# Optimization experiments

Hardware: AMD Instinct MI355X
Metric: run time of the kernel (lower is better)

## Reference

```python
import jax, jax.numpy as jnp
import numpy as np


def setup_inputs() -> dict:
    key = jax.random.key(0)
    k1, k2 = jax.random.split(key)
    num_tokens, top_k, num_experts = 1048576, 8, 64
    top_scores = jax.random.uniform(k1, (num_tokens, top_k), dtype=jnp.float32)
    selected_experts_indices = jax.random.randint(
        k2, (num_tokens, top_k), 0, num_experts, dtype=jnp.int64
    ) if jax.config.jax_enable_x64 else jax.random.randint(
        k2, (num_tokens, top_k), 0, num_experts, dtype=jnp.int32
    )
    return {
        "top_scores": top_scores,
        "selected_experts_indices": selected_experts_indices,
        "num_experts": num_experts,
    }


def reference(top_scores, selected_experts_indices, num_experts):
    flat_idx = selected_experts_indices.reshape(-1)  # [num_tokens*top_k]
    # histogram of tokens per expert (torch.histc returns float)
    num_tokens_per_expert = jnp.bincount(flat_idx, length=num_experts).astype(jnp.float32)
    # stable argsort by expert id -> permutation grouping tokens by expert
    token_indices_experts_sorted = jnp.argsort(flat_idx, stable=True)
    # gather routing scores into expert-sorted order
    top_scores_experts_sorted = top_scores.reshape(-1)[token_indices_experts_sorted]
    return (
        top_scores_experts_sorted,
        token_indices_experts_sorted,
        num_tokens_per_expert,
    )
```

## Files before the change

### kernel.cpp

```cpp
#include <hip/hip_runtime.h>


#define TILE 4096
#define WCH  1024
#define RND  16

__device__ __forceinline__ unsigned long long match_mask(
    unsigned key,
    unsigned long long b0, unsigned long long b1, unsigned long long b2,
    unsigned long long b3, unsigned long long b4, unsigned long long b5,
    unsigned long long am) {
  unsigned long long m = am;
  m &= (key & 1u)  ? b0 : ~b0;
  m &= (key & 2u)  ? b1 : ~b1;
  m &= (key & 4u)  ? b2 : ~b2;
  m &= (key & 8u)  ? b3 : ~b3;
  m &= (key & 16u) ? b4 : ~b4;
  m &= (key & 32u) ? b5 : ~b5;
  return m;
}

__global__ __launch_bounds__(256) void hist_kernel(
    const int* __restrict__ idx, unsigned* __restrict__ countsT,
    int N, int nb) {
  __shared__ unsigned h[4][64];
  const int wave = threadIdx.x >> 6;
  const int lane = threadIdx.x & 63;

  long long base = (long long)blockIdx.x * TILE;
  long long rem = (long long)N - base;
  unsigned cnt = 0;

  if (rem >= TILE) {
    const int4* v = (const int4*)(idx + base);
    unsigned es[16];
    #pragma unroll
    for (int k = 0; k < 4; ++k) {
      int4 x = v[threadIdx.x + k * 256];
      es[k * 4 + 0] = ((unsigned)x.x) & 63u;
      es[k * 4 + 1] = ((unsigned)x.y) & 63u;
      es[k * 4 + 2] = ((unsigned)x.z) & 63u;
      es[k * 4 + 3] = ((unsigned)x.w) & 63u;
    }
    #pragma unroll
    for (int r = 0; r < 16; ++r) {
      unsigned e = es[r];
      unsigned long long b0 = __ballot(e & 1u);
      unsigned long long b1 = __ballot(e & 2u);
      unsigned long long b2 = __ballot(e & 4u);
      unsigned long long b3 = __ballot(e & 8u);
      unsigned long long b4 = __ballot(e & 16u);
      unsigned long long b5 = __ballot(e & 32u);
      cnt += (unsigned)__popcll(
          match_mask((unsigned)lane, b0, b1, b2, b3, b4, b5, ~0ull));
    }
  } else {
    long long wstart = base + (long long)wave * WCH;
    for (int r = 0; r < RND; ++r) {
      long long i = wstart + (long long)r * 64 + lane;
      bool valid = i < (long long)N;
      unsigned long long am = __ballot(valid ? 1 : 0);
      unsigned e = valid ? (((unsigned)idx[i]) & 63u) : 0u;
      unsigned long long b0 = __ballot(e & 1u);
      unsigned long long b1 = __ballot(e & 2u);
      unsigned long long b2 = __ballot(e & 4u);
      unsigned long long b3 = __ballot(e & 8u);
      unsigned long long b4 = __ballot(e & 16u);
      unsigned long long b5 = __ballot(e & 32u);
      cnt += (unsigned)__popcll(
          match_mask((unsigned)lane, b0, b1, b2, b3, b4, b5, am));
    }
  }

  h[wave][lane] = cnt;
  __syncthreads();
  if (threadIdx.x < 64) {
    countsT[(size_t)blockIdx.x * 64 + threadIdx.x] =
        h[0][threadIdx.x] + h[1][threadIdx.x] + h[2][threadIdx.x] + h[3][threadIdx.x];
  }
}

__global__ __launch_bounds__(256) void scan_kernel(
    unsigned* __restrict__ countsT, unsigned* __restrict__ totals,
    float* __restrict__ out_counts, int nb) {
  const int e = blockIdx.x;
  const int t = threadIdx.x;
  const int wave = t >> 6;
  const int lane = t & 63;

  __shared__ unsigned buf[2048];
  __shared__ unsigned wsum[4];

  unsigned carry = 0;
  for (int c = 0; c < nb; c += 2048) {
    int m = nb - c; if (m > 2048) m = 2048;
    for (int j = t; j < 2048; j += 256)
      buf[j] = (j < m) ? countsT[(size_t)(c + j) * 64 + e] : 0u;
    __syncthreads();
    unsigned v[8]; unsigned s = 0;
    #pragma unroll
    for (int k = 0; k < 8; ++k) { v[k] = buf[t * 8 + k]; s += v[k]; }
    unsigned inc = s;
    #pragma unroll
    for (int d = 1; d < 64; d <<= 1) {
      unsigned nv = __shfl_up(inc, d, 64);
      if (lane >= d) inc += nv;
    }
    if (lane == 63) wsum[wave] = inc;
    __syncthreads();
    unsigned woff = 0;
    for (int w = 0; w < wave; ++w) woff += wsum[w];
    unsigned btot = wsum[0] + wsum[1] + wsum[2] + wsum[3];
    unsigned run = carry + woff + (inc - s);
    #pragma unroll
    for (int k = 0; k < 8; ++k) { buf[t * 8 + k] = run; run += v[k]; }
    __syncthreads();
    for (int j = t; j < 2048; j += 256)
      if (j < m) countsT[(size_t)(c + j) * 64 + e] = buf[j];
    carry += btot;
    __syncthreads();
  }
  if (t == 0) {
    totals[e] = carry;
    out_counts[e] = (float)carry;
  }
}

__global__ __launch_bounds__(256, 4) void scatter_kernel(
    const int* __restrict__ idx, const float* __restrict__ scores,
    const unsigned* __restrict__ baseT, const unsigned* __restrict__ totals,
    float* __restrict__ out_scores, float* __restrict__ out_idx,
    int N, int nb) {
  __shared__ __align__(16) uint2 sdat[TILE];
  __shared__ __align__(16) unsigned char tmpb[4][64][RND];
  __shared__ unsigned shc[4][64];
  __shared__ unsigned gdest[64];

  const int t = threadIdx.x;
  const int wave = t >> 6;
  const int lane = t & 63;
  const unsigned long long lt = (1ull << lane) - 1ull;

  const long long base = (long long)blockIdx.x * TILE;
  const long long start = base + (long long)wave * WCH;
  const bool fullt = (base + TILE) <= (long long)N;

  const unsigned tot = totals[lane];
  const unsigned gb0 = baseT[(size_t)blockIdx.x * 64 + lane];

  unsigned e_pk[4] = {0, 0, 0, 0};
  unsigned r_pk[4] = {0, 0, 0, 0};
  float    sreg[RND];
  unsigned c_pk[4];
  unsigned wtotal = 0;

  unsigned* idxs = (unsigned*)sdat;

  if (fullt) {
    {
      const int4* gi = (const int4*)(idx + base);
      int4 a0 = gi[t];
      int4 a1 = gi[t + 256];
      int4 a2 = gi[t + 512];
      int4 a3 = gi[t + 768];
      #pragma unroll
      for (int r = 0; r < RND; ++r) sreg[r] = scores[start + r * 64 + lane];
      ((int4*)idxs)[t] = a0;
      ((int4*)idxs)[t + 256] = a1;
      ((int4*)idxs)[t + 512] = a2;
      ((int4*)idxs)[t + 768] = a3;
    }
    *(uint4*)(&tmpb[wave][lane][0]) = make_uint4(0u, 0u, 0u, 0u);
    __syncthreads();

    #pragma unroll
    for (int r = 0; r < RND; ++r) {
      unsigned e = idxs[wave * WCH + r * 64 + lane] & 63u;
      unsigned long long b0 = __ballot(e & 1u);
      unsigned long long b1 = __ballot(e & 2u);
      unsigned long long b2 = __ballot(e & 4u);
      unsigned long long b3 = __ballot(e & 8u);
      unsigned long long b4 = __ballot(e & 16u);
      unsigned long long b5 = __ballot(e & 32u);
      unsigned long long ms = match_mask(e, b0, b1, b2, b3, b4, b5, ~0ull);
      unsigned rank = (unsigned)__popcll(ms & lt);
      unsigned rcnt = (unsigned)__popcll(ms);
      if (rank == 0) tmpb[wave][e][r] = (unsigned char)rcnt;
      const int q = r >> 2, sh = (r & 3) * 8;
      e_pk[q] |= e << sh;
      r_pk[q] |= rank << sh;
    }
    uint4 cw = *(const uint4*)(&tmpb[wave][lane][0]);
    c_pk[0] = cw.x; c_pk[1] = cw.y; c_pk[2] = cw.z; c_pk[3] = cw.w;
  } else {
    for (int j = t; j < TILE; j += 256) sdat[j].y = 0xFFFFFFFFu;
    *(uint4*)(&tmpb[wave][lane][0]) = make_uint4(0u, 0u, 0u, 0u);
    __syncthreads();
    for (int r = 0; r < RND; ++r) {
      long long i = start + (long long)r * 64 + lane;
      bool valid = i < (long long)N;
      unsigned long long am = __ballot(valid ? 1 : 0);
      unsigned e = valid ? (((unsigned)idx[i]) & 63u) : 0u;
      sreg[r] = valid ? scores[i] : 0.0f;
      unsigned long long b0 = __ballot(e & 1u);
      unsigned long long b1 = __ballot(e & 2u);
      unsigned long long b2 = __ballot(e & 4u);
      unsigned long long b3 = __ballot(e & 8u);
      unsigned long long b4 = __ballot(e & 16u);
      unsigned long long b5 = __ballot(e & 32u);
      unsigned long long ms = match_mask(e, b0, b1, b2, b3, b4, b5, am);
      unsigned rank = (unsigned)__popcll(ms & lt);
      unsigned rcnt = (unsigned)__popcll(ms);
      if (valid && rank == 0) tmpb[wave][e][r] = (unsigned char)rcnt;
      const int q = r >> 2, sh = (r & 3) * 8;
      e_pk[q] |= e << sh;
      r_pk[q] |= rank << sh;
    }
    uint4 cw = *(const uint4*)(&tmpb[wave][lane][0]);
    c_pk[0] = cw.x; c_pk[1] = cw.y; c_pk[2] = cw.z; c_pk[3] = cw.w;
  }

  {
    unsigned acc = 0;
    #pragma unroll
    for (int q = 0; q < 4; ++q)
      acc += (c_pk[q] & 0x00FF00FFu) + ((c_pk[q] >> 8) & 0x00FF00FFu);
    wtotal = (acc & 0xFFFFu) + (acc >> 16);
  }

  shc[wave][lane] = wtotal;
  __syncthreads();

  unsigned c0 = shc[0][lane], c1 = shc[1][lane];
  unsigned c2 = shc[2][lane], c3 = shc[3][lane];
  unsigned bt = c0 + c1 + c2 + c3;
  unsigned wpre = 0;
  if (wave > 0) wpre += c0;
  if (wave > 1) wpre += c1;
  if (wave > 2) wpre += c2;

  unsigned s = bt;
  #pragma unroll
  for (int d = 1; d < 64; d <<= 1) {
    unsigned nv = __shfl_up(s, d, 64);
    if (lane >= d) s += nv;
  }
  unsigned bstart = s - bt;
  unsigned wbase = bstart + wpre;

  unsigned cur[RND];
  {
    unsigned acc = wbase;
    #pragma unroll
    for (int r = 0; r < RND; ++r) {
      cur[r] = acc;
      acc += (c_pk[r >> 2] >> ((r & 3) * 8)) & 0xffu;
    }
  }

  if (wave == 0) {
    unsigned s2 = tot;
    #pragma unroll
    for (int d = 1; d < 64; d <<= 1) {
      unsigned nv = __shfl_up(s2, d, 64);
      if (lane >= d) s2 += nv;
    }
    unsigned estart = s2 - tot;
    gdest[lane] = estart + gb0 - bstart;
  }

  if (fullt) {
    #pragma unroll
    for (int r = 0; r < RND; ++r) {
      unsigned i32 = (unsigned)start + r * 64 + lane;
      const int q = r >> 2, sh = (r & 3) * 8;
      unsigned e    = (e_pk[q] >> sh) & 0xffu;
      unsigned rank = (r_pk[q] >> sh) & 0xffu;
      unsigned pos = (unsigned)__shfl((int)cur[r], (int)e, 64) + rank;
      sdat[pos] = make_uint2(__float_as_uint(sreg[r]), (i32 << 6) | e);
    }
  } else {
    for (int r = 0; r < RND; ++r) {
      long long i = start + (long long)r * 64 + lane;
      bool valid = i < (long long)N;
      const int q = r >> 2, sh = (r & 3) * 8;
      unsigned e    = (e_pk[q] >> sh) & 0xffu;
      unsigned rank = (r_pk[q] >> sh) & 0xffu;
      unsigned pos = (unsigned)__shfl((int)cur[r], (int)e, 64) + rank;
      if (valid) {
        sdat[pos] = make_uint2(__float_as_uint(sreg[r]), (((unsigned)i) << 6) | e);
      }
    }
  }
  __syncthreads();

  if (fullt) {
    #pragma unroll
    for (int k = 0; k < TILE / 256; ++k) {
      int j = t + k * 256;
      uint2 v = sdat[j];
      unsigned e = v.y & 63u;
      unsigned d = gdest[e] + (unsigned)j;
      out_scores[d] = __uint_as_float(v.x);
      out_idx[d] = (float)(v.y >> 6);
    }
  } else {
    for (int j = t; j < TILE; j += 256) {
      uint2 v = sdat[j];
      if (v.y == 0xFFFFFFFFu) continue;
      unsigned e = v.y & 63u;
      unsigned d = gdest[e] + (unsigned)j;
      out_scores[d] = __uint_as_float(v.x);
      out_idx[d] = (float)(v.y >> 6);
    }
  }
}

extern "C" void kernel_launch(void* const* d_in, const int* in_sizes, int n_in,
                              void* d_out, int out_size, void* d_ws, size_t ws_size,
                              hipStream_t stream) {
  const float* scores = (const float*)d_in[0];
  const int* idx = (const int*)d_in[1];
  int N = in_sizes[0];

  float* out_scores = (float*)d_out;
  float* out_idx = out_scores + N;
  float* out_counts = out_idx + N;

  int nb = (N + TILE - 1) / TILE;
  unsigned* countsT = (unsigned*)d_ws;
  unsigned* totals = countsT + (size_t)nb * 64;

  hist_kernel<<<nb, 256, 0, stream>>>(idx, countsT, N, nb);
  scan_kernel<<<64, 256, 0, stream>>>(countsT, totals, out_counts, nb);
  scatter_kernel<<<nb, 256, 0, stream>>>(idx, scores, countsT, totals,
                                         out_scores, out_idx, N, nb);
}
```

Before: 139.9 us.

## Gather scores at write-out instead of staging them through shared memory

The scatter kernel no longer preloads scores into registers and stages them next to indices in shared memory. The LDS tile shrinks from uint2 to unsigned per element, and launch bounds rise to 7 blocks per CU for higher occupancy. Scores are now gathered from global memory by source index during the final write-out. This replaces a coalesced score load with a scattered gather, which may cost more memory traffic than the LDS and occupancy savings recover.

Result: slower. 149.1 us (+6.6%).

```diff
diff --git a/kernel.cpp b/kernel.cpp
--- a/kernel.cpp
+++ b/kernel.cpp
@@ -126,12 +126,12 @@
   }
 }
 
-__global__ __launch_bounds__(256, 4) void scatter_kernel(
+__global__ __launch_bounds__(256, 7) void scatter_kernel(
     const int* __restrict__ idx, const float* __restrict__ scores,
     const unsigned* __restrict__ baseT, const unsigned* __restrict__ totals,
     float* __restrict__ out_scores, float* __restrict__ out_idx,
     int N, int nb) {
-  __shared__ __align__(16) uint2 sdat[TILE];
+  __shared__ __align__(16) unsigned sdat[TILE];
   __shared__ __align__(16) unsigned char tmpb[4][64][RND];
   __shared__ unsigned shc[4][64];
   __shared__ unsigned gdest[64];
@@ -150,11 +150,8 @@
 
   unsigned e_pk[4] = {0, 0, 0, 0};
   unsigned r_pk[4] = {0, 0, 0, 0};
-  float    sreg[RND];
   unsigned c_pk[4];
   unsigned wtotal = 0;
-
-  unsigned* idxs = (unsigned*)sdat;
 
   if (fullt) {
     {
@@ -163,19 +160,17 @@
       int4 a1 = gi[t + 256];
       int4 a2 = gi[t + 512];
       int4 a3 = gi[t + 768];
-      #pragma unroll
-      for (int r = 0; r < RND; ++r) sreg[r] = scores[start + r * 64 + lane];
-      ((int4*)idxs)[t] = a0;
-      ((int4*)idxs)[t + 256] = a1;
-      ((int4*)idxs)[t + 512] = a2;
-      ((int4*)idxs)[t + 768] = a3;
+      ((int4*)sdat)[t] = a0;
+      ((int4*)sdat)[t + 256] = a1;
+      ((int4*)sdat)[t + 512] = a2;
+      ((int4*)sdat)[t + 768] = a3;
     }
     *(uint4*)(&tmpb[wave][lane][0]) = make_uint4(0u, 0u, 0u, 0u);
     __syncthreads();
 
     #pragma unroll
     for (int r = 0; r < RND; ++r) {
-      unsigned e = idxs[wave * WCH + r * 64 + lane] & 63u;
+      unsigned e = sdat[wave * WCH + r * 64 + lane] & 63u;
       unsigned long long b0 = __ballot(e & 1u);
       unsigned long long b1 = __ballot(e & 2u);
       unsigned long long b2 = __ballot(e & 4u);
@@ -193,15 +188,15 @@
     uint4 cw = *(const uint4*)(&tmpb[wave][lane][0]);
     c_pk[0] = cw.x; c_pk[1] = cw.y; c_pk[2] = cw.z; c_pk[3] = cw.w;
   } else {
-    for (int j = t; j < TILE; j += 256) sdat[j].y = 0xFFFFFFFFu;
+    for (int j = t; j < TILE; j += 256) sdat[j] = 0xFFFFFFFFu;
     *(uint4*)(&tmpb[wave][lane][0]) = make_uint4(0u, 0u, 0u, 0u);
     __syncthreads();
+    unsigned epk_local[RND];
     for (int r = 0; r < RND; ++r) {
       long long i = start + (long long)r * 64 + lane;
       bool valid = i < (long long)N;
       unsigned long long am = __ballot(valid ? 1 : 0);
       unsigned e = valid ? (((unsigned)idx[i]) & 63u) : 0u;
-      sreg[r] = valid ? scores[i] : 0.0f;
       unsigned long long b0 = __ballot(e & 1u);
       unsigned long long b1 = __ballot(e & 2u);
       unsigned long long b2 = __ballot(e & 4u);
@@ -215,6 +210,7 @@
       const int q = r >> 2, sh = (r & 3) * 8;
       e_pk[q] |= e << sh;
       r_pk[q] |= rank << sh;
+      (void)epk_local;
     }
     uint4 cw = *(const uint4*)(&tmpb[wave][lane][0]);
     c_pk[0] = cw.x; c_pk[1] = cw.y; c_pk[2] = cw.z; c_pk[3] = cw.w;
@@ -277,7 +273,7 @@
       unsigned e    = (e_pk[q] >> sh) & 0xffu;
       unsigned rank = (r_pk[q] >> sh) & 0xffu;
       unsigned pos = (unsigned)__shfl((int)cur[r], (int)e, 64) + rank;
-      sdat[pos] = make_uint2(__float_as_uint(sreg[r]), (i32 << 6) | e);
+      sdat[pos] = (i32 << 6) | e;
     }
   } else {
     for (int r = 0; r < RND; ++r) {
@@ -287,31 +283,33 @@
       unsigned e    = (e_pk[q] >> sh) & 0xffu;
       unsigned rank = (r_pk[q] >> sh) & 0xffu;
       unsigned pos = (unsigned)__shfl((int)cur[r], (int)e, 64) + rank;
-      if (valid) {
-        sdat[pos] = make_uint2(__float_as_uint(sreg[r]), (((unsigned)i) << 6) | e);
-      }
+      if (valid) sdat[pos] = (((unsigned)i) << 6) | e;
     }
   }
   __syncthreads();
 
   if (fullt) {
+    unsigned vv[TILE / 256];
+    #pragma unroll
+    for (int k = 0; k < TILE / 256; ++k) vv[k] = sdat[t + k * 256];
+    float sc[TILE / 256];
+    #pragma unroll
+    for (int k = 0; k < TILE / 256; ++k) sc[k] = scores[vv[k] >> 6];
     #pragma unroll
     for (int k = 0; k < TILE / 256; ++k) {
       int j = t + k * 256;
-      uint2 v = sdat[j];
-      unsigned e = v.y & 63u;
-      unsigned d = gdest[e] + (unsigned)j;
-      out_scores[d] = __uint_as_float(v.x);
-      out_idx[d] = (float)(v.y >> 6);
+      unsigned v = vv[k];
+      unsigned d = gdest[v & 63u] + (unsigned)j;
+      out_scores[d] = sc[k];
+      out_idx[d] = (float)(v >> 6);
     }
   } else {
     for (int j = t; j < TILE; j += 256) {
-      uint2 v = sdat[j];
-      if (v.y == 0xFFFFFFFFu) continue;
-      unsigned e = v.y & 63u;
-      unsigned d = gdest[e] + (unsigned)j;
-      out_scores[d] = __uint_as_float(v.x);
-      out_idx[d] = (float)(v.y >> 6);
+      unsigned v = sdat[j];
+      if (v == 0xFFFFFFFFu) continue;
+      unsigned d = gdest[v & 63u] + (unsigned)j;
+      out_scores[d] = scores[v >> 6];
+      out_idx[d] = (float)(v >> 6);
     }
   }
 }
```
